# Optimization experiments

Hardware: AMD Instinct MI355X
Metric: run time of the kernel (lower is better)

## Reference

```python
import jax, jax.numpy as jnp
import numpy as np
import math

H = 32          # num heads
D_NOPE = 128
D_ROPE = 64
D_QK = D_NOPE + D_ROPE   # 192
D_V = 128
KV_LORA = 512
EPS = 1e-6
ROPE_THETA = 10000.0
FACTOR = 40.0
BETA_FAST, BETA_SLOW = 32.0, 1.0
ORIG_MAX_POS = 4096
MSCALE_ALL_DIM = 1.0


def _yarn_inv_freq():
    dim = D_ROPE
    pos_freqs = ROPE_THETA ** (np.arange(0, dim, 2, dtype=np.float64) / dim)
    inv_extra = 1.0 / pos_freqs
    inv_inter = 1.0 / (FACTOR * pos_freqs)

    def corr_dim(n_rot):
        return dim * math.log(ORIG_MAX_POS / (n_rot * 2 * math.pi)) / (2 * math.log(ROPE_THETA))
    low = max(math.floor(corr_dim(BETA_FAST)), 0)
    high = min(math.ceil(corr_dim(BETA_SLOW)), dim - 1)
    ramp = np.clip((np.arange(dim // 2, dtype=np.float64) - low) / max(high - low, 1e-3), 0, 1)
    inv_freq_mask = 1.0 - ramp  # extrapolation_factor = 1
    inv_freq = inv_inter * (1 - inv_freq_mask) + inv_extra * inv_freq_mask
    return jnp.asarray(inv_freq, dtype=jnp.float32)  # [D_ROPE//2]


def _apply_rope_gptj(x, cos, sin):
    # x: [T, n, D_ROPE]; cos/sin: [T, D_ROPE//2]; interleaved (is_neox_style=False)
    x2 = x.reshape(*x.shape[:-1], D_ROPE // 2, 2)
    x1, xo = x2[..., 0], x2[..., 1]
    c = cos[:, None, :]
    s = sin[:, None, :]
    r1 = x1 * c - xo * s
    r2 = xo * c + x1 * s
    return jnp.stack([r1, r2], axis=-1).reshape(x.shape)


def _rmsnorm(x, w):
    var = jnp.mean(x.astype(jnp.float32) ** 2, axis=-1, keepdims=True)
    return (x * jax.lax.rsqrt(var + EPS)) * w


def setup_inputs() -> dict:
    key = jax.random.key(0)
    ks = jax.random.split(key, 8)
    T, HID = 2048, 4096
    def w(k, shape, fan_in):
        return jax.random.normal(k, shape, dtype=jnp.float32) * (1.0 / math.sqrt(fan_in))
    return {
        "positions": jnp.arange(T, dtype=jnp.int32),
        "hidden_states": jax.random.normal(ks[0], (T, HID), dtype=jnp.float32),
        "Wqa": w(ks[1], (HID, 1536), HID),
        "q_a_ln": jnp.ones((1536,), dtype=jnp.float32),
        "Wqb": w(ks[2], (1536, H * D_QK), 1536),
        "Wkva": w(ks[3], (HID, KV_LORA + D_ROPE), HID),
        "kv_a_ln": jnp.ones((KV_LORA,), dtype=jnp.float32),
        "Wkvb": w(ks[4], (KV_LORA, H * (D_NOPE + D_V)), KV_LORA),
        "Wo": w(ks[5], (H * D_V, HID), H * D_V),
    }


def reference(positions, hidden_states, Wqa, q_a_ln, Wqb, Wkva, kv_a_ln, Wkvb, Wo):
    T = hidden_states.shape[0]
    # softmax scaling with yarn mscale correction
    mscale = 0.1 * MSCALE_ALL_DIM * math.log(FACTOR) + 1.0
    scaling = (D_QK ** -0.5) * mscale * mscale

    # --- low-rank Q path ---
    q = hidden_states @ Wqa                       # [T, 1536]
    q = _rmsnorm(q, q_a_ln)
    q = (q @ Wqb).reshape(T, H, D_QK)             # [T, H, 192]
    q_nope, q_pe = q[..., :D_NOPE], q[..., D_NOPE:]

    # --- low-rank latent KV path ---
    latent = hidden_states @ Wkva                 # [T, 576]
    kv_a = _rmsnorm(latent[:, :KV_LORA], kv_a_ln) # [T, 512]
    k_pe = latent[:, None, KV_LORA:]              # [T, 1, 64]
    kv = (kv_a @ Wkvb).reshape(T, H, D_NOPE + D_V)
    k_nope = kv[..., :D_NOPE]                     # [T, H, 128]
    v = kv[..., D_NOPE:]                          # [T, H, 128]

    # --- decoupled RoPE on rope slice only ---
    inv_freq = _yarn_inv_freq()
    freqs = positions.astype(jnp.float32)[:, None] * inv_freq[None, :]  # [T, 32]
    cos, sin = jnp.cos(freqs), jnp.sin(freqs)
    q_pe = _apply_rope_gptj(q_pe, cos, sin)       # [T, H, 64]
    k_pe = _apply_rope_gptj(k_pe, cos, sin)       # [T, 1, 64]

    q = jnp.concatenate([q_nope, q_pe], axis=-1)                      # [T, H, 192]
    k = jnp.concatenate([k_nope, jnp.broadcast_to(k_pe, (T, H, D_ROPE))], axis=-1)

    # --- causal MHA over assembled K/V ---
    scores = jnp.einsum('thd,shd->hts', q, k) * scaling               # [H, T, T]
    causal = positions[None, :, None] >= positions[None, None, :]
    scores = jnp.where(causal, scores, jnp.finfo(scores.dtype).min)
    probs = jax.nn.softmax(scores, axis=-1)
    attn = jnp.einsum('hts,shd->thd', probs, v).reshape(T, H * D_V)
    return attn @ Wo                                                   # [T, 4096]
```

## Files before the change

kernel.cpp:

```cpp
#include <hip/hip_runtime.h>
#include <math.h>

typedef __bf16 bf16x8 __attribute__((ext_vector_type(8)));
typedef float f32x4 __attribute__((ext_vector_type(4)));
typedef unsigned short u16;
typedef unsigned int u32;

#define T_SEQ 2048
#define NHEAD 32

__device__ __forceinline__ u16 f2bu(float f){
  u32 u = __float_as_uint(f);
  u32 r = (u + 0x7fffu + ((u >> 16) & 1u)) >> 16;
  return (u16)r;
}

__device__ __forceinline__ void gload_lds16(const void* g, void* l){
  __builtin_amdgcn_global_load_lds((const __attribute__((address_space(1))) u32*)g,
                                   (__attribute__((address_space(3))) u32*)l, 16, 0, 0);
}

__global__ void cast_f32_bf16(const float* __restrict__ in, u16* __restrict__ out, int n4){
  int i = blockIdx.x * blockDim.x + threadIdx.x;
  int stride = gridDim.x * blockDim.x;
  for (; i < n4; i += stride){
    float4 v = ((const float4*)in)[i];
    ushort4 o;
    o.x = f2bu(v.x); o.y = f2bu(v.y); o.z = f2bu(v.z); o.w = f2bu(v.w);
    ((ushort4*)out)[i] = o;
  }
}

__device__ __forceinline__ void tc_body(const float* __restrict__ src, u16* __restrict__ dst,
                                        int K, int N, int k0, int n0){
  __shared__ float tile[64][65];
  int t = threadIdx.x;
  int rr = t >> 4, c4 = (t & 15) * 4;
  #pragma unroll
  for (int i = 0; i < 4; i++){
    int r = rr + i * 16;
    int n = n0 + c4;
    float4 v;
    if (n < N) v = *(const float4*)(src + (size_t)(k0 + r) * N + n);
    else       v = make_float4(0.f, 0.f, 0.f, 0.f);
    tile[r][c4]     = v.x;
    tile[r][c4 + 1] = v.y;
    tile[r][c4 + 2] = v.z;
    tile[r][c4 + 3] = v.w;
  }
  __syncthreads();
  #pragma unroll
  for (int i = 0; i < 4; i++){
    int n = rr + i * 16;
    ushort4 o;
    o.x = f2bu(tile[c4 + 0][n]);
    o.y = f2bu(tile[c4 + 1][n]);
    o.z = f2bu(tile[c4 + 2][n]);
    o.w = f2bu(tile[c4 + 3][n]);
    *(ushort4*)(dst + (size_t)(n0 + n) * K + k0 + c4) = o;
  }
}

__global__ __launch_bounds__(256) void transpose_batch(
    const float* __restrict__ Wqa, u16* __restrict__ WqaT,
    const float* __restrict__ Wkva, u16* __restrict__ WkvaT,
    const float* __restrict__ Wqb, u16* __restrict__ WqbT,
    const float* __restrict__ Wkvb, u16* __restrict__ WkvbT,
    const float* __restrict__ Wo, u16* __restrict__ WoT){
  int bid = blockIdx.x;
  const float* s; u16* d; int K, N, gx, l;
  if (bid < 1536)      { s = Wqa;  d = WqaT;  K = 4096; N = 1536; gx = 64; l = bid; }
  else if (bid < 2176) { s = Wkva; d = WkvaT; K = 4096; N = 576;  gx = 64; l = bid - 1536; }
  else if (bid < 4480) { s = Wqb;  d = WqbT;  K = 1536; N = 6144; gx = 24; l = bid - 2176; }
  else if (bid < 5504) { s = Wkvb; d = WkvbT; K = 512;  N = 8192; gx = 8;  l = bid - 4480; }
  else                 { s = Wo;   d = WoT;   K = 4096; N = 4096; gx = 64; l = bid - 5504; }
  tc_body(s, d, K, N, (l % gx) * 64, (l / gx) * 64);
}

__global__ void rope_table(const int* __restrict__ positions, float* __restrict__ cosT,
                           float* __restrict__ sinT, float lo, float denom){
  int idx = blockIdx.x * blockDim.x + threadIdx.x;
  if (idx >= T_SEQ * 32) return;
  int t = idx >> 5, i = idx & 31;
  float pf = powf(10000.f, (float)i / 32.f);
  float inv_extra = 1.f / pf;
  float inv_inter = 1.f / (40.f * pf);
  float ramp = fminf(fmaxf(((float)i - lo) / denom, 0.f), 1.f);
  float invf = inv_inter * ramp + inv_extra * (1.f - ramp);
  float fr = (float)positions[t] * invf;
  cosT[idx] = cosf(fr);
  sinT[idx] = sinf(fr);
}

__global__ void rmsnorm_cast(const float* __restrict__ in, int istride, int n,
                             const float* __restrict__ w, u16* __restrict__ out, int ostride){
  int row = blockIdx.x;
  const float* x = in + (size_t)row * istride;
  float ss = 0.f;
  for (int c = threadIdx.x; c < n; c += blockDim.x){ float v = x[c]; ss += v * v; }
  #pragma unroll
  for (int off = 1; off < 64; off <<= 1) ss += __shfl_xor(ss, off);
  __shared__ float wsum[4];
  if ((threadIdx.x & 63) == 0) wsum[threadIdx.x >> 6] = ss;
  __syncthreads();
  float tot = wsum[0] + wsum[1] + wsum[2] + wsum[3];
  float scale = rsqrtf(tot / (float)n + 1e-6f);
  for (int c = threadIdx.x; c < n; c += blockDim.x)
    out[(size_t)row * ostride + c] = f2bu(x[c] * scale * w[c]);
}

__global__ void rope_kpe(const float* __restrict__ lat, int lstride, int loff,
                         const float* __restrict__ cosT,
                         const float* __restrict__ sinT, u16* __restrict__ kpe){
  int idx = blockIdx.x * blockDim.x + threadIdx.x;
  if (idx >= T_SEQ * 32) return;
  int t = idx >> 5, i = idx & 31;
  float x1 = lat[(size_t)t * lstride + loff + 2 * i];
  float x2 = lat[(size_t)t * lstride + loff + 2 * i + 1];
  float c = cosT[idx], s = sinT[idx];
  kpe[t * 64 + 2 * i]     = f2bu(x1 * c - x2 * s);
  kpe[t * 64 + 2 * i + 1] = f2bu(x2 * c + x1 * s);
}

template<int EPI>
__global__ __launch_bounds__(256) void gemm_bt(const u16* __restrict__ A, const u16* __restrict__ BT,
                                               float* __restrict__ C, u16* __restrict__ O1,
                                               u16* __restrict__ O2,
                                               const float* __restrict__ cosT,
                                               const float* __restrict__ sinT,
                                               float scaling, int M, int N, int K){
  __shared__ __align__(1024) char lds[32768];
  const int tid = threadIdx.x;
  const int wave = tid >> 6, lane = tid & 63;
  const int lg = lane >> 4, lm = lane & 15;

  int gx = gridDim.x;
  int nwg = gx * gridDim.y;
  int orig = blockIdx.y * gx + blockIdx.x;
  int qq = nwg >> 3, rr_ = nwg & 7, xc = orig & 7, rest = orig >> 3;
  int wg = (xc < rr_ ? xc * (qq + 1) : rr_ * (qq + 1) + (xc - rr_) * qq) + rest;
  const int bn = (wg % gx) * 128, bm = (wg / gx) * 128;

  const int wr = (wave >> 1) * 64, wc = (wave & 1) * 64;
  f32x4 acc[4][4] = {};
  int srow[2], scol[2], soff[2];
  #pragma unroll
  for (int j = 0; j < 2; j++){
    int o = (wave * 2 + j) * 1024 + lane * 16;
    int row = o >> 6;
    int cg = ((o >> 4) & 3) ^ ((row >> 1) & 3);
    srow[j] = row; scol[j] = cg * 8; soff[j] = (wave * 2 + j) * 1024;
  }

  #pragma unroll
  for (int j = 0; j < 2; j++){
    gload_lds16(A  + (size_t)(bm + srow[j]) * K + scol[j], lds + soff[j]);
    gload_lds16(BT + (size_t)(bn + srow[j]) * K + scol[j], lds + 16384 + soff[j]);
  }

  int cur = 0;
  for (int k0 = 0; k0 < K; k0 += 32){
    if (k0 + 32 < K){
      char* dA = lds + (cur ^ 1) * 8192;
      char* dB = lds + 16384 + (cur ^ 1) * 8192;
      #pragma unroll
      for (int j = 0; j < 2; j++){
        gload_lds16(A  + (size_t)(bm + srow[j]) * K + k0 + 32 + scol[j], dA + soff[j]);
        gload_lds16(BT + (size_t)(bn + srow[j]) * K + k0 + 32 + scol[j], dB + soff[j]);
      }
      asm volatile("s_waitcnt vmcnt(4)" ::: "memory");
    } else {
      asm volatile("s_waitcnt vmcnt(0)" ::: "memory");
    }
    __builtin_amdgcn_sched_barrier(0);
    __builtin_amdgcn_s_barrier();

    const char* ldsA = lds + cur * 8192;
    const char* ldsB = lds + 16384 + cur * 8192;
    bf16x8 af[4], bfr[4];
    #pragma unroll
    for (int m = 0; m < 4; m++){
      int r = wr + m * 16 + lm;
      af[m] = *(const bf16x8*)(ldsA + r * 64 + ((lg ^ ((r >> 1) & 3)) << 4));
    }
    #pragma unroll
    for (int n = 0; n < 4; n++){
      int r = wc + n * 16 + lm;
      bfr[n] = *(const bf16x8*)(ldsB + r * 64 + ((lg ^ ((r >> 1) & 3)) << 4));
    }
    __builtin_amdgcn_s_setprio(1);
    #pragma unroll
    for (int m = 0; m < 4; m++)
      #pragma unroll
      for (int n = 0; n < 4; n++)
        acc[m][n] = __builtin_amdgcn_mfma_f32_16x16x32_bf16(af[m], bfr[n], acc[m][n], 0, 0, 0);
    __builtin_amdgcn_s_setprio(0);
    __builtin_amdgcn_s_barrier();
    cur ^= 1;
  }

  #pragma unroll
  for (int m = 0; m < 4; m++)
    #pragma unroll
    for (int n = 0; n < 4; n++){
      const int r0 = bm + wr + m * 16 + lg * 4;
      const int c  = bn + wc + n * 16 + lm;
      if (EPI == 0){
        #pragma unroll
        for (int q = 0; q < 4; q++)
          C[(size_t)(r0 + q) * N + c] = acc[m][n][q];
      } else if (EPI == 1){
        #pragma unroll
        for (int q = 0; q < 4; q++){
          float v = acc[m][n][q];
          float vp = __shfl_xor(v, 1);
          int h = c / 192, d = c - h * 192;
          float outv;
          if (d < 128) outv = v;
          else {
            int i = (d - 128) >> 1;
            float co = cosT[(r0 + q) * 32 + i], si = sinT[(r0 + q) * 32 + i];
            outv = (d & 1) ? (v * co + vp * si) : (v * co - vp * si);
          }
          O1[(size_t)h * T_SEQ * 192 + (size_t)(r0 + q) * 192 + d] = f2bu(outv * scaling);
        }
      } else {
        int h = c >> 8, d = c & 255;
        if (d < 128){
          #pragma unroll
          for (int q = 0; q < 4; q++)
            O1[(size_t)h * T_SEQ * 128 + (size_t)(r0 + q) * 128 + d] = f2bu(acc[m][n][q]);
        } else {
          ushort4 o;
          o.x = f2bu(acc[m][n][0]); o.y = f2bu(acc[m][n][1]);
          o.z = f2bu(acc[m][n][2]); o.w = f2bu(acc[m][n][3]);
          *(ushort4*)(O2 + (size_t)(h * 128 + (d - 128)) * T_SEQ + r0) = o;
        }
      }
    }
}

__global__ __launch_bounds__(512, 4) void flash_attn(const u16* __restrict__ Qp, const u16* __restrict__ Kp,
                                                     const u16* __restrict__ kpe, const u16* __restrict__ Vt,
                                                     u16* __restrict__ attnb){
  const int b = blockIdx.x;
  const int h = (b & 7) + 8 * ((b >> 3) & 3);
  const int qt = (b < 256) ? (15 - (b >> 5)) : ((b - 256) >> 5);
  const int tid = threadIdx.x;
  const int wave = tid >> 6, lane = tid & 63;
  const int lg = lane >> 4, lm = lane & 15;
  const int qbase = qt * 128 + wave * 16;

  __shared__ __align__(1024) char lds[51200];
  u16* Pw = (u16*)(lds + 40960 + wave * 1280);

  const u16* KpH = Kp + (size_t)h * T_SEQ * 128;
  const u16* VtH = Vt + (size_t)h * 128 * T_SEQ;

  int kO[2], kLoc[2], kPE[2];
  #pragma unroll
  for (int j = 0; j < 2; j++){
    int o = tid + 512 * j;
    int r = (o / 24) & 31, c = o % 24;
    int cx = c ^ (r & 7);
    kO[j] = o * 16;
    if (cx < 16){ kPE[j] = 0; kLoc[j] = r * 128 + cx * 8; }
    else        { kPE[j] = 1; kLoc[j] = r * 64 + (cx - 16) * 8; }
  }
  int vO, vSrc;
  { int o = tid; int d = o >> 2, c = o & 3; vO = o * 16; vSrc = d * T_SEQ + ((c ^ ((d >> 1) & 3)) << 3); }

  #define STAGE_KV(t, bi)                                                              \
    do {                                                                               \
      char* _k = lds + (bi) * 12288;                                                   \
      char* _v = lds + 24576 + (bi) * 8192;                                            \
      { const u16* _s = kPE[0] ? (kpe + (size_t)(t) * 2048 + kLoc[0])                  \
                               : (KpH + (size_t)(t) * 4096 + kLoc[0]);                 \
        gload_lds16(_s, _k + kO[0]); }                                                 \
      if (tid < 256){                                                                  \
        const u16* _s = kPE[1] ? (kpe + (size_t)(t) * 2048 + kLoc[1])                  \
                               : (KpH + (size_t)(t) * 4096 + kLoc[1]);                 \
        gload_lds16(_s, _k + kO[1]); }                                                 \
      gload_lds16(VtH + vSrc + (t) * 32, _v + vO);                                     \
    } while (0)

  const int nt = 4 * qt + 4;

  bf16x8 qf[6];
  const u16* Qbase = Qp + (size_t)(h * T_SEQ + qbase + lm) * 192 + lg * 8;
  #pragma unroll
  for (int dk = 0; dk < 6; dk++) qf[dk] = *(const bf16x8*)(Qbase + dk * 32);

  f32x4 o_[8] = {};
  float m_[4], l_[4];
  #pragma unroll
  for (int q = 0; q < 4; q++){ m_[q] = -3.0e38f; l_[q] = 0.f; }

  STAGE_KV(0, 0);

  #pragma unroll 1
  for (int kt = 0; kt < nt; kt++){
    const int t0 = kt * 32;
    const int bsel = kt & 1;
    asm volatile("s_waitcnt vmcnt(0)" ::: "memory");
    __builtin_amdgcn_sched_barrier(0);
    __builtin_amdgcn_s_barrier();
    if (kt + 1 < nt) STAGE_KV(kt + 1, bsel ^ 1);
    const char* Kb = lds + bsel * 12288;
    const char* Vb = lds + 24576 + bsel * 8192;

    f32x4 s_[2] = {};
    __builtin_amdgcn_s_setprio(1);
    #pragma unroll
    for (int hh = 0; hh < 2; hh++){
      const int r = hh * 16 + lm;
      const int rb = r * 384, rx = r & 7;
      #pragma unroll
      for (int dk = 0; dk < 6; dk++){
        bf16x8 kf = *(const bf16x8*)(Kb + rb + (((dk * 4 + lg) ^ rx) << 4));
        s_[hh] = __builtin_amdgcn_mfma_f32_16x16x32_bf16(qf[dk], kf, s_[hh], 0, 0, 0);
      }
    }
    __builtin_amdgcn_s_setprio(0);
    if (kt + 4 >= nt){
      #pragma unroll
      for (int hh = 0; hh < 2; hh++)
        #pragma unroll
        for (int q = 0; q < 4; q++){
          int col = t0 + hh * 16 + lm;
          int qrow = qbase + lg * 4 + q;
          if (col > qrow) s_[hh][q] = -3.0e38f;
        }
    }
    float pm[4];
    #pragma unroll
    for (int q = 0; q < 4; q++) pm[q] = fmaxf(s_[0][q], s_[1][q]);
    int ok = (pm[0] <= m_[0] + 8.f) & (pm[1] <= m_[1] + 8.f) &
             (pm[2] <= m_[2] + 8.f) & (pm[3] <= m_[3] + 8.f);
    if (!__all(ok)){
      #pragma unroll
      for (int q = 0; q < 4; q++){
        float v = pm[q];
        #pragma unroll
        for (int off = 8; off; off >>= 1) v = fmaxf(v, __shfl_xor(v, off));
        float mn = fmaxf(m_[q], v);
        float alpha = (m_[q] <= -1.0e37f) ? 0.f : exp2f(m_[q] - mn);
        l_[q] *= alpha;
        #pragma unroll
        for (int n = 0; n < 8; n++) o_[n][q] *= alpha;
        m_[q] = mn;
      }
    }
    #pragma unroll
    for (int q = 0; q < 4; q++){
      #pragma unroll
      for (int hh = 0; hh < 2; hh++){
        float p = exp2f(s_[hh][q] - m_[q]);
        l_[q] += p;
        ((__bf16*)Pw)[(lg * 4 + q) * 40 + hh * 16 + lm] = (__bf16)p;
      }
    }
    asm volatile("s_waitcnt lgkmcnt(0)" ::: "memory");
    __builtin_amdgcn_sched_barrier(0);
    bf16x8 pf = *(const bf16x8*)((const char*)Pw + lm * 80 + lg * 16);
    __builtin_amdgcn_s_setprio(1);
    #pragma unroll
    for (int n = 0; n < 8; n++){
      const int d = n * 16 + lm;
      bf16x8 vf = *(const bf16x8*)(Vb + d * 64 + ((lg ^ ((d >> 1) & 3)) << 4));
      o_[n] = __builtin_amdgcn_mfma_f32_16x16x32_bf16(pf, vf, o_[n], 0, 0, 0);
    }
    __builtin_amdgcn_s_setprio(0);
  }

  #pragma unroll
  for (int q = 0; q < 4; q++){
    #pragma unroll
    for (int off = 8; off; off >>= 1) l_[q] += __shfl_xor(l_[q], off);
  }
  float inv[4];
  #pragma unroll
  for (int q = 0; q < 4; q++) inv[q] = 1.f / l_[q];
  #pragma unroll
  for (int n = 0; n < 8; n++)
    #pragma unroll
    for (int q = 0; q < 4; q++){
      int r = qbase + lg * 4 + q;
      ((__bf16*)attnb)[(size_t)r * 4096 + h * 128 + n * 16 + lm] = (__bf16)(o_[n][q] * inv[q]);
    }
  #undef STAGE_KV
}

extern "C" void kernel_launch(void* const* d_in, const int* in_sizes, int n_in,
                              void* d_out, int out_size, void* d_ws, size_t ws_size,
                              hipStream_t stream){
  const int*   positions = (const int*)d_in[0];
  const float* hidden    = (const float*)d_in[1];
  const float* Wqa       = (const float*)d_in[2];
  const float* q_a_ln    = (const float*)d_in[3];
  const float* Wqb       = (const float*)d_in[4];
  const float* Wkva      = (const float*)d_in[5];
  const float* kv_a_ln   = (const float*)d_in[6];
  const float* Wkvb      = (const float*)d_in[7];
  const float* Wo        = (const float*)d_in[8];
  float* out = (float*)d_out;
  char* ws = (char*)d_ws;

  const size_t o_hidB  = 0;
  const size_t o_cos   = 16777216;
  const size_t o_sin   = 17039360;
  const size_t o_kpe   = 17301504;
  const size_t o_comb  = 17563648;
  const size_t o_qln   = 35389440;
  const size_t o_kva   = 41680896;
  const size_t o_WqaT  = 43778048;
  const size_t o_WkvaT = 56360960;
  const size_t o_WqbT  = 61603840;
  const size_t o_WkvbT = 80478208;
  const size_t o_Qp    = 88866816;
  const size_t o_Kp    = 114032640;
  const size_t o_Vt    = 147587072;
  const size_t o_WoT   = 164364288;

  u16*   hidB  = (u16*)(ws + o_hidB);
  u16*   attnb = (u16*)(ws + o_hidB);
  float* cosT  = (float*)(ws + o_cos);
  float* sinT  = (float*)(ws + o_sin);
  u16*   kpe   = (u16*)(ws + o_kpe);
  float* comb  = (float*)(ws + o_comb);
  u16*   qln   = (u16*)(ws + o_qln);
  u16*   kva   = (u16*)(ws + o_kva);
  u16*   WqaT  = (u16*)(ws + o_WqaT);
  u16*   WkvaT = (u16*)(ws + o_WkvaT);
  u16*   WqbT  = (u16*)(ws + o_WqbT);
  u16*   WkvbT = (u16*)(ws + o_WkvbT);
  u16*   Qp    = (u16*)(ws + o_Qp);
  u16*   Kp    = (u16*)(ws + o_Kp);
  u16*   Vt    = (u16*)(ws + o_Vt);
  u16*   WoT   = (u16*)(ws + o_WoT);

  double mscale = 0.1 * log(40.0) + 1.0;
  double scaling_d = pow(192.0, -0.5) * mscale * mscale;
  float scaling_log2 = (float)(scaling_d * 1.4426950408889634);
  const double PI = 3.14159265358979323846;
  double cd_fast = 64.0 * log(4096.0 / (32.0 * 2.0 * PI)) / (2.0 * log(10000.0));
  double cd_slow = 64.0 * log(4096.0 / ( 1.0 * 2.0 * PI)) / (2.0 * log(10000.0));
  double lo_d = fmax(floor(cd_fast), 0.0);
  double hi_d = fmin(ceil(cd_slow), 63.0);
  float lo = (float)lo_d;
  float denom = (float)fmax(hi_d - lo_d, 0.001);

  transpose_batch<<<9600, 256, 0, stream>>>(Wqa, WqaT, Wkva, WkvaT, Wqb, WqbT,
                                            Wkvb, WkvbT, Wo, WoT);
  cast_f32_bf16<<<2048, 256, 0, stream>>>(hidden, hidB, T_SEQ * 4096 / 4);
  rope_table<<<256, 256, 0, stream>>>(positions, cosT, sinT, lo, denom);
  gemm_bt<0><<<dim3(2176 / 128, 2048 / 128), 256, 0, stream>>>(hidB, WqaT, comb, nullptr, nullptr,
                                                               nullptr, nullptr, 0.f, 2048, 2176, 4096);
  rmsnorm_cast<<<2048, 256, 0, stream>>>(comb, 2176, 1536, q_a_ln, qln, 1536);
  rmsnorm_cast<<<2048, 256, 0, stream>>>(comb + 1536, 2176, 512, kv_a_ln, kva, 512);
  rope_kpe<<<256, 256, 0, stream>>>(comb, 2176, 2048, cosT, sinT, kpe);
  gemm_bt<1><<<dim3(6144 / 128, 2048 / 128), 256, 0, stream>>>(qln, WqbT, nullptr, Qp, nullptr,
                                                               cosT, sinT, scaling_log2, 2048, 6144, 1536);
  gemm_bt<2><<<dim3(8192 / 128, 2048 / 128), 256, 0, stream>>>(kva, WkvbT, nullptr, Kp, Vt,
                                                               nullptr, nullptr, 0.f, 2048, 8192, 512);
  flash_attn<<<512, 512, 0, stream>>>(Qp, Kp, kpe, Vt, attnb);
  gemm_bt<0><<<dim3(4096 / 128, 2048 / 128), 256, 0, stream>>>(attnb, WoT, out, nullptr, nullptr,
                                                               nullptr, nullptr, 0.f, 2048, 4096, 4096);
}
```

Measured before the change: 396.9 us.

## Merge preprocessing kernels and group Q/KV up-projection GEMMs into single launches

Weight transposes, the hidden-state cast and the RoPE table now run in one kernel, dispatched by block index instead of three launches. The Q up-projection and KV up-projection GEMMs become one grouped GEMM launch that picks operands and epilogue per workgroup segment. This cuts launch overhead and lets the short-K KV tiles fill in alongside the Q tiles, reducing tail idle time. The cost is more branching and register pressure in the shared GEMM template.

```diff
diff --git a/kernel.cpp b/kernel.cpp
--- a/kernel.cpp
+++ b/kernel.cpp
@@ -18,17 +18,6 @@
 __device__ __forceinline__ void gload_lds16(const void* g, void* l){
   __builtin_amdgcn_global_load_lds((const __attribute__((address_space(1))) u32*)g,
                                    (__attribute__((address_space(3))) u32*)l, 16, 0, 0);
-}
-
-__global__ void cast_f32_bf16(const float* __restrict__ in, u16* __restrict__ out, int n4){
-  int i = blockIdx.x * blockDim.x + threadIdx.x;
-  int stride = gridDim.x * blockDim.x;
-  for (; i < n4; i += stride){
-    float4 v = ((const float4*)in)[i];
-    ushort4 o;
-    o.x = f2bu(v.x); o.y = f2bu(v.y); o.z = f2bu(v.z); o.w = f2bu(v.w);
-    ((ushort4*)out)[i] = o;
-  }
 }
 
 __device__ __forceinline__ void tc_body(const float* __restrict__ src, u16* __restrict__ dst,
@@ -61,35 +50,46 @@
   }
 }
 
-__global__ __launch_bounds__(256) void transpose_batch(
+__global__ __launch_bounds__(256) void pre_batch(
     const float* __restrict__ Wqa, u16* __restrict__ WqaT,
     const float* __restrict__ Wkva, u16* __restrict__ WkvaT,
     const float* __restrict__ Wqb, u16* __restrict__ WqbT,
     const float* __restrict__ Wkvb, u16* __restrict__ WkvbT,
-    const float* __restrict__ Wo, u16* __restrict__ WoT){
+    const float* __restrict__ Wo, u16* __restrict__ WoT,
+    const float* __restrict__ hidden, u16* __restrict__ hidB,
+    const int* __restrict__ positions, float* __restrict__ cosT,
+    float* __restrict__ sinT, float lo, float denom){
   int bid = blockIdx.x;
-  const float* s; u16* d; int K, N, gx, l;
-  if (bid < 1536)      { s = Wqa;  d = WqaT;  K = 4096; N = 1536; gx = 64; l = bid; }
-  else if (bid < 2176) { s = Wkva; d = WkvaT; K = 4096; N = 576;  gx = 64; l = bid - 1536; }
-  else if (bid < 4480) { s = Wqb;  d = WqbT;  K = 1536; N = 6144; gx = 24; l = bid - 2176; }
-  else if (bid < 5504) { s = Wkvb; d = WkvbT; K = 512;  N = 8192; gx = 8;  l = bid - 4480; }
-  else                 { s = Wo;   d = WoT;   K = 4096; N = 4096; gx = 64; l = bid - 5504; }
-  tc_body(s, d, K, N, (l % gx) * 64, (l / gx) * 64);
-}
-
-__global__ void rope_table(const int* __restrict__ positions, float* __restrict__ cosT,
-                           float* __restrict__ sinT, float lo, float denom){
-  int idx = blockIdx.x * blockDim.x + threadIdx.x;
-  if (idx >= T_SEQ * 32) return;
-  int t = idx >> 5, i = idx & 31;
-  float pf = powf(10000.f, (float)i / 32.f);
-  float inv_extra = 1.f / pf;
-  float inv_inter = 1.f / (40.f * pf);
-  float ramp = fminf(fmaxf(((float)i - lo) / denom, 0.f), 1.f);
-  float invf = inv_inter * ramp + inv_extra * (1.f - ramp);
-  float fr = (float)positions[t] * invf;
-  cosT[idx] = cosf(fr);
-  sinT[idx] = sinf(fr);
+  if (bid < 9600){
+    const float* s; u16* d; int K, N, gx, l;
+    if (bid < 1536)      { s = Wqa;  d = WqaT;  K = 4096; N = 1536; gx = 64; l = bid; }
+    else if (bid < 2176) { s = Wkva; d = WkvaT; K = 4096; N = 576;  gx = 64; l = bid - 1536; }
+    else if (bid < 4480) { s = Wqb;  d = WqbT;  K = 1536; N = 6144; gx = 24; l = bid - 2176; }
+    else if (bid < 5504) { s = Wkvb; d = WkvbT; K = 512;  N = 8192; gx = 8;  l = bid - 4480; }
+    else                 { s = Wo;   d = WoT;   K = 4096; N = 4096; gx = 64; l = bid - 5504; }
+    tc_body(s, d, K, N, (l % gx) * 64, (l / gx) * 64);
+  } else if (bid < 11648){
+    int l = bid - 9600;
+    #pragma unroll
+    for (int i = 0; i < 4; i++){
+      int idx = l * 1024 + threadIdx.x + i * 256;
+      float4 v = ((const float4*)hidden)[idx];
+      ushort4 o;
+      o.x = f2bu(v.x); o.y = f2bu(v.y); o.z = f2bu(v.z); o.w = f2bu(v.w);
+      ((ushort4*)hidB)[idx] = o;
+    }
+  } else {
+    int idx = (bid - 11648) * 256 + threadIdx.x;
+    int t = idx >> 5, i = idx & 31;
+    float pf = powf(10000.f, (float)i / 32.f);
+    float inv_extra = 1.f / pf;
+    float inv_inter = 1.f / (40.f * pf);
+    float ramp = fminf(fmaxf(((float)i - lo) / denom, 0.f), 1.f);
+    float invf = inv_inter * ramp + inv_extra * (1.f - ramp);
+    float fr = (float)positions[t] * invf;
+    cosT[idx] = cosf(fr);
+    sinT[idx] = sinf(fr);
+  }
 }
 
 __global__ void rmsnorm_cast(const float* __restrict__ in, int istride, int n,
@@ -124,8 +124,10 @@
 
 template<int EPI>
 __global__ __launch_bounds__(256) void gemm_bt(const u16* __restrict__ A, const u16* __restrict__ BT,
-                                               float* __restrict__ C, u16* __restrict__ O1,
-                                               u16* __restrict__ O2,
+                                               float* __restrict__ C,
+                                               u16* __restrict__ O1, u16* __restrict__ O2,
+                                               u16* __restrict__ O3,
+                                               const u16* __restrict__ A2, const u16* __restrict__ BT2,
                                                const float* __restrict__ cosT,
                                                const float* __restrict__ sinT,
                                                float scaling, int M, int N, int K){
@@ -139,7 +141,15 @@
   int orig = blockIdx.y * gx + blockIdx.x;
   int qq = nwg >> 3, rr_ = nwg & 7, xc = orig & 7, rest = orig >> 3;
   int wg = (xc < rr_ ? xc * (qq + 1) : rr_ * (qq + 1) + (xc - rr_) * qq) + rest;
-  const int bn = (wg % gx) * 128, bm = (wg / gx) * 128;
+
+  const u16* Ap; const u16* BTp; int Kv, bn, bm, seg = 0;
+  if constexpr (EPI == 3){
+    if (wg < 768){ seg = 0; Ap = A;  BTp = BT;  Kv = 1536; bn = (wg % 48) * 128; bm = (wg / 48) * 128; }
+    else         { seg = 1; Ap = A2; BTp = BT2; Kv = 512;  int l2 = wg - 768; bn = (l2 & 63) * 128; bm = (l2 >> 6) * 128; }
+  } else {
+    Ap = A; BTp = BT; Kv = K;
+    bn = (wg % gx) * 128; bm = (wg / gx) * 128;
+  }
 
   const int wr = (wave >> 1) * 64, wc = (wave & 1) * 64;
   f32x4 acc[4][4] = {};
@@ -154,19 +164,19 @@
 
   #pragma unroll
   for (int j = 0; j < 2; j++){
-    gload_lds16(A  + (size_t)(bm + srow[j]) * K + scol[j], lds + soff[j]);
-    gload_lds16(BT + (size_t)(bn + srow[j]) * K + scol[j], lds + 16384 + soff[j]);
+    gload_lds16(Ap  + (size_t)(bm + srow[j]) * Kv + scol[j], lds + soff[j]);
+    gload_lds16(BTp + (size_t)(bn + srow[j]) * Kv + scol[j], lds + 16384 + soff[j]);
   }
 
   int cur = 0;
-  for (int k0 = 0; k0 < K; k0 += 32){
-    if (k0 + 32 < K){
+  for (int k0 = 0; k0 < Kv; k0 += 32){
+    if (k0 + 32 < Kv){
       char* dA = lds + (cur ^ 1) * 8192;
       char* dB = lds + 16384 + (cur ^ 1) * 8192;
       #pragma unroll
       for (int j = 0; j < 2; j++){
-        gload_lds16(A  + (size_t)(bm + srow[j]) * K + k0 + 32 + scol[j], dA + soff[j]);
-        gload_lds16(BT + (size_t)(bn + srow[j]) * K + k0 + 32 + scol[j], dB + soff[j]);
+        gload_lds16(Ap  + (size_t)(bm + srow[j]) * Kv + k0 + 32 + scol[j], dA + soff[j]);
+        gload_lds16(BTp + (size_t)(bn + srow[j]) * Kv + k0 + 32 + scol[j], dB + soff[j]);
       }
       asm volatile("s_waitcnt vmcnt(4)" ::: "memory");
     } else {
@@ -209,32 +219,34 @@
         #pragma unroll
         for (int q = 0; q < 4; q++)
           C[(size_t)(r0 + q) * N + c] = acc[m][n][q];
-      } else if (EPI == 1){
-        #pragma unroll
-        for (int q = 0; q < 4; q++){
-          float v = acc[m][n][q];
-          float vp = __shfl_xor(v, 1);
-          int h = c / 192, d = c - h * 192;
-          float outv;
-          if (d < 128) outv = v;
-          else {
-            int i = (d - 128) >> 1;
-            float co = cosT[(r0 + q) * 32 + i], si = sinT[(r0 + q) * 32 + i];
-            outv = (d & 1) ? (v * co + vp * si) : (v * co - vp * si);
+      } else {
+        if (seg == 0){
+          #pragma unroll
+          for (int q = 0; q < 4; q++){
+            float v = acc[m][n][q];
+            float vp = __shfl_xor(v, 1);
+            int h = c / 192, d = c - h * 192;
+            float outv;
+            if (d < 128) outv = v;
+            else {
+              int i = (d - 128) >> 1;
+              float co = cosT[(r0 + q) * 32 + i], si = sinT[(r0 + q) * 32 + i];
+              outv = (d & 1) ? (v * co + vp * si) : (v * co - vp * si);
+            }
+            O1[(size_t)h * T_SEQ * 192 + (size_t)(r0 + q) * 192 + d] = f2bu(outv * scaling);
           }
-          O1[(size_t)h * T_SEQ * 192 + (size_t)(r0 + q) * 192 + d] = f2bu(outv * scaling);
-        }
-      } else {
-        int h = c >> 8, d = c & 255;
-        if (d < 128){
-          #pragma unroll
-          for (int q = 0; q < 4; q++)
-            O1[(size_t)h * T_SEQ * 128 + (size_t)(r0 + q) * 128 + d] = f2bu(acc[m][n][q]);
         } else {
-          ushort4 o;
-          o.x = f2bu(acc[m][n][0]); o.y = f2bu(acc[m][n][1]);
-          o.z = f2bu(acc[m][n][2]); o.w = f2bu(acc[m][n][3]);
-          *(ushort4*)(O2 + (size_t)(h * 128 + (d - 128)) * T_SEQ + r0) = o;
+          int h = c >> 8, d = c & 255;
+          if (d < 128){
+            #pragma unroll
+            for (int q = 0; q < 4; q++)
+              O2[(size_t)h * T_SEQ * 128 + (size_t)(r0 + q) * 128 + d] = f2bu(acc[m][n][q]);
+          } else {
+            ushort4 o;
+            o.x = f2bu(acc[m][n][0]); o.y = f2bu(acc[m][n][1]);
+            o.z = f2bu(acc[m][n][2]); o.w = f2bu(acc[m][n][3]);
+            *(ushort4*)(O3 + (size_t)(h * 128 + (d - 128)) * T_SEQ + r0) = o;
+          }
         }
       }
     }
@@ -450,20 +462,19 @@
   float lo = (float)lo_d;
   float denom = (float)fmax(hi_d - lo_d, 0.001);
 
-  transpose_batch<<<9600, 256, 0, stream>>>(Wqa, WqaT, Wkva, WkvaT, Wqb, WqbT,
-                                            Wkvb, WkvbT, Wo, WoT);
-  cast_f32_bf16<<<2048, 256, 0, stream>>>(hidden, hidB, T_SEQ * 4096 / 4);
-  rope_table<<<256, 256, 0, stream>>>(positions, cosT, sinT, lo, denom);
-  gemm_bt<0><<<dim3(2176 / 128, 2048 / 128), 256, 0, stream>>>(hidB, WqaT, comb, nullptr, nullptr,
-                                                               nullptr, nullptr, 0.f, 2048, 2176, 4096);
+  pre_batch<<<11904, 256, 0, stream>>>(Wqa, WqaT, Wkva, WkvaT, Wqb, WqbT, Wkvb, WkvbT,
+                                       Wo, WoT, hidden, hidB, positions, cosT, sinT, lo, denom);
+  gemm_bt<0><<<dim3(2176 / 128, 2048 / 128), 256, 0, stream>>>(
+      hidB, WqaT, comb, nullptr, nullptr, nullptr, nullptr, nullptr,
+      nullptr, nullptr, 0.f, 2048, 2176, 4096);
   rmsnorm_cast<<<2048, 256, 0, stream>>>(comb, 2176, 1536, q_a_ln, qln, 1536);
   rmsnorm_cast<<<2048, 256, 0, stream>>>(comb + 1536, 2176, 512, kv_a_ln, kva, 512);
   rope_kpe<<<256, 256, 0, stream>>>(comb, 2176, 2048, cosT, sinT, kpe);
-  gemm_bt<1><<<dim3(6144 / 128, 2048 / 128), 256, 0, stream>>>(qln, WqbT, nullptr, Qp, nullptr,
-                                                               cosT, sinT, scaling_log2, 2048, 6144, 1536);
-  gemm_bt<2><<<dim3(8192 / 128, 2048 / 128), 256, 0, stream>>>(kva, WkvbT, nullptr, Kp, Vt,
-                                                               nullptr, nullptr, 0.f, 2048, 8192, 512);
+  gemm_bt<3><<<1792, 256, 0, stream>>>(
+      qln, WqbT, nullptr, Qp, Kp, Vt, kva, WkvbT,
+      cosT, sinT, scaling_log2, 0, 0, 0);
   flash_attn<<<512, 512, 0, stream>>>(Qp, Kp, kpe, Vt, attnb);
-  gemm_bt<0><<<dim3(4096 / 128, 2048 / 128), 256, 0, stream>>>(attnb, WoT, out, nullptr, nullptr,
-                                                               nullptr, nullptr, 0.f, 2048, 4096, 4096);
-}
+  gemm_bt<0><<<dim3(4096 / 128, 2048 / 128), 256, 0, stream>>>(
+      attnb, WoT, out, nullptr, nullptr, nullptr, nullptr, nullptr,
+      nullptr, nullptr, 0.f, 2048, 4096, 4096);
+}
```

After: 444.7 us. 1.12x slower.
